# Performance work log

Measured on AMD Instinct MI355X. Metric: run time of the kernel, lower is better.

## Reference

```python
import jax, jax.numpy as jnp
import numpy as np

N_NODES = 50000
N_EDGES = 800000
IN_DIM, HID, EMB = 128, 256, 128


def _gcn_conv(x, src, dst, W, b, n_nodes):
    # PyG GCNConv: add self-loops, symmetric norm D^-1/2 (A+I) D^-1/2, then linear.
    h = x @ W  # [N, out]
    deg = jnp.zeros((n_nodes,), x.dtype).at[dst].add(1.0) + 1.0  # +1 for self-loop
    dinv = jax.lax.rsqrt(deg)
    norm = dinv[src] * dinv[dst]  # [E]
    agg = jnp.zeros_like(h).at[dst].add(h[src] * norm[:, None])
    agg = agg + h * (dinv * dinv)[:, None]  # self-loop term
    return agg + b


def setup_inputs() -> dict:
    key = jax.random.key(0)
    ks = jax.random.split(key, 16)
    s = lambda *sh: None
    x = jax.random.normal(ks[0], (N_NODES, IN_DIM), jnp.float32)
    edge_index = jax.random.randint(ks[1], (2, N_EDGES), 0, N_NODES, jnp.int32)
    def lin(k, fan_in, fan_out):
        lim = 1.0 / np.sqrt(fan_in)
        kw, kb = jax.random.split(k)
        W = jax.random.uniform(kw, (fan_in, fan_out), jnp.float32, -lim, lim)
        b = jax.random.uniform(kb, (fan_out,), jnp.float32, -lim, lim)
        return W, b
    W1, b1 = lin(ks[2], IN_DIM, HID)
    W2, b2 = lin(ks[3], HID, EMB)
    fc1_W, fc1_b = lin(ks[4], EMB, HID)
    fc2_W, fc2_b = lin(ks[5], HID, 1)
    np_W, np_b = lin(ks[6], EMB, 3)
    ep_W, ep_b = lin(ks[7], 2 * EMB, 2)
    gp_W, gp_b = lin(ks[8], EMB, 1)
    return dict(x=x, edge_index=edge_index, W1=W1, b1=b1, W2=W2, b2=b2,
                fc1_W=fc1_W, fc1_b=fc1_b, fc2_W=fc2_W, fc2_b=fc2_b,
                np_W=np_W, np_b=np_b, ep_W=ep_W, ep_b=ep_b, gp_W=gp_W, gp_b=gp_b)


def reference(x, edge_index, W1, b1, W2, b2, fc1_W, fc1_b, fc2_W, fc2_b,
              np_W, np_b, ep_W, ep_b, gp_W, gp_b):
    src, dst = edge_index[0], edge_index[1]
    n = x.shape[0]
    h = jax.nn.relu(_gcn_conv(x, src, dst, W1, b1, n))
    h = jax.nn.relu(_gcn_conv(h, src, dst, W2, b2, n))  # [N, EMB]
    g = jnp.mean(h, axis=0, keepdims=True)  # [1, EMB]
    v = jax.nn.relu(g @ fc1_W + fc1_b)
    value = v @ fc2_W + fc2_b  # [1,1]
    node_logits = h @ np_W + np_b  # [N,3]
    edge_features = jnp.concatenate([h[src], h[dst]], axis=1)  # [E, 2*EMB]
    edge_logits = edge_features @ ep_W + ep_b  # [E,2]
    global_logits = g @ gp_W + gp_b  # [1,1]
    return (node_logits, edge_logits, global_logits, value)
```

## Files before the change

kernel.cpp:

```cpp
#include <hip/hip_runtime.h>
#include <hip/hip_bf16.h>

typedef __attribute__((ext_vector_type(8))) short bf16x8;
typedef __attribute__((ext_vector_type(4))) float f32x4;

__device__ inline unsigned short f2bf(float f) {
    union { float f; unsigned u; } v; v.f = f;
    unsigned r = v.u + 0x7fff + ((v.u >> 16) & 1);
    return (unsigned short)(r >> 16);
}
__device__ inline float bf2f(unsigned short b) {
    union { unsigned u; float f; } v; v.u = ((unsigned)b) << 16;
    return v.f;
}
__device__ inline float bfu_lo(unsigned r) {
    union { unsigned u; float f; } v; v.u = r << 16;
    return v.f;
}
__device__ inline float bfu_hi(unsigned r) {
    union { unsigned u; float f; } v; v.u = r & 0xffff0000u;
    return v.f;
}

__global__ __launch_bounds__(256) void prep_kernel(
    const float* __restrict__ x, unsigned short* __restrict__ xb,
    const float* __restrict__ W1, unsigned short* __restrict__ W1t_hi, unsigned short* __restrict__ W1t_lo,
    const float* __restrict__ W2, unsigned short* __restrict__ W2t_hi, unsigned short* __restrict__ W2t_lo,
    int* __restrict__ zero_ints, float* __restrict__ gsum, int n) {
    int tid = blockIdx.x * blockDim.x + threadIdx.x;
    int C = n * 32;
    if (tid < C) {
        int base = tid * 4;
        float4 v = *(const float4*)&x[base];
        unsigned lo = (unsigned)f2bf(v.x) | ((unsigned)f2bf(v.y) << 16);
        unsigned hi = (unsigned)f2bf(v.z) | ((unsigned)f2bf(v.w) << 16);
        uint2 p; p.x = lo; p.y = hi;
        *(uint2*)&xb[base] = p;
        return;
    }
    tid -= C;
    if (tid < 65536) {
        if (tid < 32768) {
            int k = tid >> 8, j = tid & 255;
            float v = W1[tid];
            unsigned short h = f2bf(v);
            W1t_hi[(size_t)j * 128 + k] = h;
            W1t_lo[(size_t)j * 128 + k] = f2bf(v - bf2f(h));
        } else {
            int i2 = tid - 32768;
            int k = i2 >> 7, j = i2 & 127;
            float v = W2[i2];
            unsigned short h = f2bf(v);
            W2t_hi[(size_t)j * 256 + k] = h;
            W2t_lo[(size_t)j * 256 + k] = f2bf(v - bf2f(h));
        }
        return;
    }
    tid -= 65536;
    if (tid < 2 * n) { zero_ints[tid] = 0; return; }
    tid -= 2 * n;
    if (tid < 128) gsum[tid] = 0.f;
}

__global__ void hist_kernel(const int* __restrict__ dst, int* __restrict__ deg, int nE) {
    int e = blockIdx.x * blockDim.x + threadIdx.x;
    if (e < nE) atomicAdd(&deg[dst[e]], 1);
}

__global__ __launch_bounds__(1024) void scanA_kernel(const int* __restrict__ deg,
                                                     int* __restrict__ local,
                                                     float* __restrict__ dinv,
                                                     int* __restrict__ bsum, int n) {
    __shared__ int wsum[16];
    __shared__ int woff[16];
    int t = threadIdx.x, lane = t & 63, wid = t >> 6;
    int i = blockIdx.x * 1024 + t;
    int val = (i < n) ? deg[i] : 0;
    if (i < n) dinv[i] = rsqrtf((float)(val + 1));
    int inc = val;
    for (int s = 1; s < 64; s <<= 1) {
        int tmp = __shfl_up(inc, s);
        if (lane >= s) inc += tmp;
    }
    if (lane == 63) wsum[wid] = inc;
    __syncthreads();
    if (wid == 0) {
        int w = (lane < 16) ? wsum[lane] : 0;
        for (int s = 1; s < 16; s <<= 1) {
            int tmp = __shfl_up(w, s);
            if (lane >= s) w += tmp;
        }
        if (lane < 16) woff[lane] = w - wsum[lane];
        if (lane == 15) bsum[blockIdx.x] = w;
    }
    __syncthreads();
    if (i < n) local[i] = woff[wid] + (inc - val);
}

__global__ void scanB_kernel(const int* __restrict__ bsum, int* __restrict__ boff, int nb) {
    int lane = threadIdx.x & 63;
    int v = (lane < nb) ? bsum[lane] : 0;
    int inc = v;
    for (int s = 1; s < 64; s <<= 1) {
        int tmp = __shfl_up(inc, s);
        if (lane >= s) inc += tmp;
    }
    if (lane < nb) boff[lane] = inc - v;
}

__global__ void fill_kernel(const int* __restrict__ src, const int* __restrict__ dst,
                            const int* __restrict__ local, const int* __restrict__ boff,
                            int* __restrict__ cnt, const float* __restrict__ dinv,
                            int2* __restrict__ csr, int nE) {
    int e = blockIdx.x * blockDim.x + threadIdx.x;
    if (e >= nE) return;
    int s = src[e], d = dst[e];
    int pos = local[d] + boff[d >> 10] + atomicAdd(&cnt[d], 1);
    float w = dinv[s] * dinv[d];
    csr[pos] = make_int2(s, __float_as_int(w));
}

__global__ __launch_bounds__(256) void gather1_kernel(const unsigned int* __restrict__ xb,
                                                      const int2* __restrict__ csr,
                                                      const int* __restrict__ local,
                                                      const int* __restrict__ boff,
                                                      const int* __restrict__ deg,
                                                      const float* __restrict__ dinv,
                                                      unsigned int* __restrict__ xin_hi,
                                                      unsigned int* __restrict__ xin_lo, int n) {
    int node = blockIdx.x * 4 + (threadIdx.x >> 6);
    int lane = threadIdx.x & 63;
    if (node >= n) return;
    int p = local[node] + boff[node >> 10];
    int e0 = p + deg[node];
    unsigned rs = xb[(size_t)node * 64 + lane];
    float a0 = 0.f, a1 = 0.f, b0 = 0.f, b1 = 0.f;
    float c0 = 0.f, c1 = 0.f, d0v = 0.f, d1v = 0.f;
    for (; p + 7 < e0; p += 8) {
        int2 q0 = csr[p], q1 = csr[p + 1], q2 = csr[p + 2], q3 = csr[p + 3];
        int2 q4 = csr[p + 4], q5 = csr[p + 5], q6 = csr[p + 6], q7 = csr[p + 7];
        unsigned r0 = xb[(size_t)q0.x * 64 + lane];
        unsigned r1 = xb[(size_t)q1.x * 64 + lane];
        unsigned r2 = xb[(size_t)q2.x * 64 + lane];
        unsigned r3 = xb[(size_t)q3.x * 64 + lane];
        unsigned r4 = xb[(size_t)q4.x * 64 + lane];
        unsigned r5 = xb[(size_t)q5.x * 64 + lane];
        unsigned r6 = xb[(size_t)q6.x * 64 + lane];
        unsigned r7 = xb[(size_t)q7.x * 64 + lane];
        float w0 = __int_as_float(q0.y), w1 = __int_as_float(q1.y);
        float w2 = __int_as_float(q2.y), w3 = __int_as_float(q3.y);
        float w4 = __int_as_float(q4.y), w5 = __int_as_float(q5.y);
        float w6 = __int_as_float(q6.y), w7 = __int_as_float(q7.y);
        a0 += w0 * bfu_lo(r0); a1 += w0 * bfu_hi(r0);
        b0 += w1 * bfu_lo(r1); b1 += w1 * bfu_hi(r1);
        c0 += w2 * bfu_lo(r2); c1 += w2 * bfu_hi(r2);
        d0v += w3 * bfu_lo(r3); d1v += w3 * bfu_hi(r3);
        a0 += w4 * bfu_lo(r4); a1 += w4 * bfu_hi(r4);
        b0 += w5 * bfu_lo(r5); b1 += w5 * bfu_hi(r5);
        c0 += w6 * bfu_lo(r6); c1 += w6 * bfu_hi(r6);
        d0v += w7 * bfu_lo(r7); d1v += w7 * bfu_hi(r7);
    }
    for (; p + 3 < e0; p += 4) {
        int2 q0 = csr[p], q1 = csr[p + 1], q2 = csr[p + 2], q3 = csr[p + 3];
        unsigned r0 = xb[(size_t)q0.x * 64 + lane];
        unsigned r1 = xb[(size_t)q1.x * 64 + lane];
        unsigned r2 = xb[(size_t)q2.x * 64 + lane];
        unsigned r3 = xb[(size_t)q3.x * 64 + lane];
        float w0 = __int_as_float(q0.y), w1 = __int_as_float(q1.y);
        float w2 = __int_as_float(q2.y), w3 = __int_as_float(q3.y);
        a0 += w0 * bfu_lo(r0); a1 += w0 * bfu_hi(r0);
        b0 += w1 * bfu_lo(r1); b1 += w1 * bfu_hi(r1);
        c0 += w2 * bfu_lo(r2); c1 += w2 * bfu_hi(r2);
        d0v += w3 * bfu_lo(r3); d1v += w3 * bfu_hi(r3);
    }
    for (; p < e0; ++p) {
        int2 q = csr[p];
        float w = __int_as_float(q.y);
        unsigned r = xb[(size_t)q.x * 64 + lane];
        a0 += w * bfu_lo(r); a1 += w * bfu_hi(r);
    }
    a0 = (a0 + b0) + (c0 + d0v);
    a1 = (a1 + b1) + (c1 + d1v);
    float di = dinv[node];
    float d2 = di * di;
    a0 += d2 * bfu_lo(rs);
    a1 += d2 * bfu_hi(rs);
    unsigned short h0 = f2bf(a0), h1 = f2bf(a1);
    xin_hi[(size_t)node * 64 + lane] = (unsigned)h0 | ((unsigned)h1 << 16);
    unsigned short l0 = f2bf(a0 - bf2f(h0)), l1 = f2bf(a1 - bf2f(h1));
    xin_lo[(size_t)node * 64 + lane] = (unsigned)l0 | ((unsigned)l1 << 16);
}

template <int K, int NOUT, bool BIAS_RELU, bool A_SPLIT>
__global__ __launch_bounds__(256) void mfma_gemm_kernel(
    const unsigned short* __restrict__ Ahi, const unsigned short* __restrict__ Alo,
    const unsigned short* __restrict__ Wthi, const unsigned short* __restrict__ Wtlo,
    const float* __restrict__ bias,
    unsigned short* __restrict__ O, int n) {
    int w = threadIdx.x >> 6, l = threadIdx.x & 63;
    int m0 = blockIdx.x * 128 + w * 32;
    int j0 = blockIdx.y * 64;
    int col16 = l & 15;
    int koff = (l >> 4) * 8;
    int rowA0 = m0 + col16;       if (rowA0 >= n) rowA0 = n - 1;
    int rowA1 = m0 + 16 + col16;  if (rowA1 >= n) rowA1 = n - 1;
    f32x4 acc[2][4];
#pragma unroll
    for (int g = 0; g < 2; ++g)
#pragma unroll
        for (int c = 0; c < 4; ++c) acc[g][c] = (f32x4){0.f, 0.f, 0.f, 0.f};
    for (int k0 = 0; k0 < K; k0 += 32) {
        bf16x8 ah0 = *(const bf16x8*)&Ahi[(size_t)rowA0 * K + k0 + koff];
        bf16x8 ah1 = *(const bf16x8*)&Ahi[(size_t)rowA1 * K + k0 + koff];
        bf16x8 al0, al1;
        if (A_SPLIT) {
            al0 = *(const bf16x8*)&Alo[(size_t)rowA0 * K + k0 + koff];
            al1 = *(const bf16x8*)&Alo[(size_t)rowA1 * K + k0 + koff];
        }
#pragma unroll
        for (int c = 0; c < 4; ++c) {
            size_t wb = (size_t)(j0 + c * 16 + col16) * K + k0 + koff;
            bf16x8 wh = *(const bf16x8*)&Wthi[wb];
            bf16x8 wl = *(const bf16x8*)&Wtlo[wb];
            acc[0][c] = __builtin_amdgcn_mfma_f32_16x16x32_bf16(ah0, wh, acc[0][c], 0, 0, 0);
            if (A_SPLIT) acc[0][c] = __builtin_amdgcn_mfma_f32_16x16x32_bf16(al0, wh, acc[0][c], 0, 0, 0);
            acc[0][c] = __builtin_amdgcn_mfma_f32_16x16x32_bf16(ah0, wl, acc[0][c], 0, 0, 0);
            acc[1][c] = __builtin_amdgcn_mfma_f32_16x16x32_bf16(ah1, wh, acc[1][c], 0, 0, 0);
            if (A_SPLIT) acc[1][c] = __builtin_amdgcn_mfma_f32_16x16x32_bf16(al1, wh, acc[1][c], 0, 0, 0);
            acc[1][c] = __builtin_amdgcn_mfma_f32_16x16x32_bf16(ah1, wl, acc[1][c], 0, 0, 0);
        }
    }
#pragma unroll
    for (int g = 0; g < 2; ++g) {
#pragma unroll
        for (int c = 0; c < 4; ++c) {
            int col = j0 + c * 16 + col16;
#pragma unroll
            for (int r = 0; r < 4; ++r) {
                int orow = m0 + g * 16 + (l >> 4) * 4 + r;
                if (orow >= n) continue;
                float v = acc[g][c][r];
                if (BIAS_RELU) v = fmaxf(v + bias[col], 0.f);
                O[(size_t)orow * NOUT + col] = f2bf(v);
            }
        }
    }
}

__global__ __launch_bounds__(256) void conv2_fused_kernel(
    const unsigned int* __restrict__ h2b, const int2* __restrict__ csr,
    const int* __restrict__ local, const int* __restrict__ boff,
    const int* __restrict__ deg,
    const float* __restrict__ dinv, const float* __restrict__ b2,
    const float* __restrict__ npW, const float* __restrict__ npb,
    const float* __restrict__ epW, const float* __restrict__ epb,
    float* __restrict__ out_nl, float* __restrict__ uv,
    float* __restrict__ gsum, int n) {
    __shared__ float lgs[4][128];
    int lane = threadIdx.x & 63;
    int wid = threadIdx.x >> 6;
    int d0 = lane * 2, d1 = lane * 2 + 1;
    float wn00 = npW[d0 * 3 + 0], wn10 = npW[d0 * 3 + 1], wn20 = npW[d0 * 3 + 2];
    float wn01 = npW[d1 * 3 + 0], wn11 = npW[d1 * 3 + 1], wn21 = npW[d1 * 3 + 2];
    float wu00 = epW[d0 * 2 + 0], wu10 = epW[d0 * 2 + 1];
    float wu01 = epW[d1 * 2 + 0], wu11 = epW[d1 * 2 + 1];
    float wv00 = epW[(d0 + 128) * 2 + 0], wv10 = epW[(d0 + 128) * 2 + 1];
    float wv01 = epW[(d1 + 128) * 2 + 0], wv11 = epW[(d1 + 128) * 2 + 1];
    float b20 = b2[d0], b21 = b2[d1];
    float npb0 = npb[0], npb1 = npb[1], npb2 = npb[2];
    float epb0 = epb[0], epb1 = epb[1];
    float p0 = 0.f, p1 = 0.f;

    for (int node = blockIdx.x * 4 + wid; node < n; node += gridDim.x * 4) {
        int p = local[node] + boff[node >> 10];
        int e0 = p + deg[node];
        unsigned rs = h2b[(size_t)node * 64 + lane];
        float a0 = 0.f, a1 = 0.f, b0 = 0.f, b1 = 0.f;
        float c0 = 0.f, c1 = 0.f, e0v = 0.f, e1v = 0.f;
        for (; p + 7 < e0; p += 8) {
            int2 q0 = csr[p], q1 = csr[p + 1], q2 = csr[p + 2], q3 = csr[p + 3];
            int2 q4 = csr[p + 4], q5 = csr[p + 5], q6 = csr[p + 6], q7 = csr[p + 7];
            unsigned r0 = h2b[(size_t)q0.x * 64 + lane];
            unsigned r1 = h2b[(size_t)q1.x * 64 + lane];
            unsigned r2 = h2b[(size_t)q2.x * 64 + lane];
            unsigned r3 = h2b[(size_t)q3.x * 64 + lane];
            unsigned r4 = h2b[(size_t)q4.x * 64 + lane];
            unsigned r5 = h2b[(size_t)q5.x * 64 + lane];
            unsigned r6 = h2b[(size_t)q6.x * 64 + lane];
            unsigned r7 = h2b[(size_t)q7.x * 64 + lane];
            float w0 = __int_as_float(q0.y), w1 = __int_as_float(q1.y);
            float w2 = __int_as_float(q2.y), w3 = __int_as_float(q3.y);
            float w4 = __int_as_float(q4.y), w5 = __int_as_float(q5.y);
            float w6 = __int_as_float(q6.y), w7 = __int_as_float(q7.y);
            a0 += w0 * bfu_lo(r0); a1 += w0 * bfu_hi(r0);
            b0 += w1 * bfu_lo(r1); b1 += w1 * bfu_hi(r1);
            c0 += w2 * bfu_lo(r2); c1 += w2 * bfu_hi(r2);
            e0v += w3 * bfu_lo(r3); e1v += w3 * bfu_hi(r3);
            a0 += w4 * bfu_lo(r4); a1 += w4 * bfu_hi(r4);
            b0 += w5 * bfu_lo(r5); b1 += w5 * bfu_hi(r5);
            c0 += w6 * bfu_lo(r6); c1 += w6 * bfu_hi(r6);
            e0v += w7 * bfu_lo(r7); e1v += w7 * bfu_hi(r7);
        }
        for (; p + 3 < e0; p += 4) {
            int2 q0 = csr[p], q1 = csr[p + 1], q2 = csr[p + 2], q3 = csr[p + 3];
            unsigned r0 = h2b[(size_t)q0.x * 64 + lane];
            unsigned r1 = h2b[(size_t)q1.x * 64 + lane];
            unsigned r2 = h2b[(size_t)q2.x * 64 + lane];
            unsigned r3 = h2b[(size_t)q3.x * 64 + lane];
            float w0 = __int_as_float(q0.y), w1 = __int_as_float(q1.y);
            float w2 = __int_as_float(q2.y), w3 = __int_as_float(q3.y);
            a0 += w0 * bfu_lo(r0); a1 += w0 * bfu_hi(r0);
            b0 += w1 * bfu_lo(r1); b1 += w1 * bfu_hi(r1);
            c0 += w2 * bfu_lo(r2); c1 += w2 * bfu_hi(r2);
            e0v += w3 * bfu_lo(r3); e1v += w3 * bfu_hi(r3);
        }
        for (; p < e0; ++p) {
            int2 q = csr[p];
            float w = __int_as_float(q.y);
            unsigned r = h2b[(size_t)q.x * 64 + lane];
            a0 += w * bfu_lo(r); a1 += w * bfu_hi(r);
        }
        a0 = (a0 + b0) + (c0 + e0v);
        a1 = (a1 + b1) + (c1 + e1v);
        float di = dinv[node];
        float d2 = di * di;
        a0 = fmaxf(a0 + d2 * bfu_lo(rs) + b20, 0.f);
        a1 = fmaxf(a1 + d2 * bfu_hi(rs) + b21, 0.f);
        p0 += a0;
        p1 += a1;
        float n0 = a0 * wn00 + a1 * wn01;
        float n1 = a0 * wn10 + a1 * wn11;
        float n2 = a0 * wn20 + a1 * wn21;
        float u0 = a0 * wu00 + a1 * wu01;
        float u1 = a0 * wu10 + a1 * wu11;
        float v0 = a0 * wv00 + a1 * wv01;
        float v1 = a0 * wv10 + a1 * wv11;
        for (int off = 32; off; off >>= 1) {
            n0 += __shfl_xor(n0, off);
            n1 += __shfl_xor(n1, off);
            n2 += __shfl_xor(n2, off);
            u0 += __shfl_xor(u0, off);
            u1 += __shfl_xor(u1, off);
            v0 += __shfl_xor(v0, off);
            v1 += __shfl_xor(v1, off);
        }
        if (lane == 0) {
            out_nl[(size_t)node * 3 + 0] = n0 + npb0;
            out_nl[(size_t)node * 3 + 1] = n1 + npb1;
            out_nl[(size_t)node * 3 + 2] = n2 + npb2;
            float4 o;
            o.x = u0 + epb0; o.y = u1 + epb1; o.z = v0; o.w = v1;
            *(float4*)&uv[(size_t)node * 4] = o;
        }
    }
    lgs[wid][d0] = p0;
    lgs[wid][d1] = p1;
    __syncthreads();
    int t = threadIdx.x;
    if (t < 128) {
        float tot = lgs[0][t] + lgs[1][t] + lgs[2][t] + lgs[3][t];
        atomicAdd(&gsum[t], tot);
    }
}

__global__ __launch_bounds__(256) void edge_head_kernel(
    const float* __restrict__ uv, const int* __restrict__ src, const int* __restrict__ dst,
    float* __restrict__ out_el, int nE,
    const float* __restrict__ gsum,
    const float* __restrict__ fc1W, const float* __restrict__ fc1b,
    const float* __restrict__ fc2W, const float* __restrict__ fc2b,
    const float* __restrict__ gpW, const float* __restrict__ gpb,
    float* __restrict__ out_gl, float* __restrict__ out_val, int n) {
    if (blockIdx.x == 0) {
        __shared__ float g[128];
        __shared__ float red[256];
        int t = threadIdx.x;
        if (t < 128) g[t] = gsum[t] * (1.0f / (float)n);
        __syncthreads();
        float v = fc1b[t];
#pragma unroll
        for (int k = 0; k < 128; ++k) v += g[k] * fc1W[k * 256 + t];
        v = fmaxf(v, 0.0f);
        red[t] = v * fc2W[t];
        __syncthreads();
        for (int s = 128; s > 0; s >>= 1) { if (t < s) red[t] += red[t + s]; __syncthreads(); }
        if (t == 0) out_val[0] = red[0] + fc2b[0];
        __syncthreads();
        red[t] = (t < 128) ? g[t] * gpW[t] : 0.0f;
        __syncthreads();
        for (int s = 128; s > 0; s >>= 1) { if (t < s) red[t] += red[t + s]; __syncthreads(); }
        if (t == 0) out_gl[0] = red[0] + gpb[0];
        return;
    }
    int e = (blockIdx.x - 1) * blockDim.x + threadIdx.x;
    if (e >= nE) return;
    int s = src[e], d = dst[e];
    float2 u = *(const float2*)&uv[(size_t)s * 4];
    float2 v = *(const float2*)&uv[(size_t)d * 4 + 2];
    float2 o; o.x = u.x + v.x; o.y = u.y + v.y;
    *(float2*)&out_el[(size_t)e * 2] = o;
}

extern "C" void kernel_launch(void* const* d_in, const int* in_sizes, int n_in,
                              void* d_out, int out_size, void* d_ws, size_t ws_size,
                              hipStream_t stream) {
    const float* x    = (const float*)d_in[0];
    const int*   ei   = (const int*)d_in[1];
    const float* W1   = (const float*)d_in[2];
    const float* b1   = (const float*)d_in[3];
    const float* W2   = (const float*)d_in[4];
    const float* b2   = (const float*)d_in[5];
    const float* fc1W = (const float*)d_in[6];
    const float* fc1b = (const float*)d_in[7];
    const float* fc2W = (const float*)d_in[8];
    const float* fc2b = (const float*)d_in[9];
    const float* npW  = (const float*)d_in[10];
    const float* npb  = (const float*)d_in[11];
    const float* epW  = (const float*)d_in[12];
    const float* epb  = (const float*)d_in[13];
    const float* gpW  = (const float*)d_in[14];
    const float* gpb  = (const float*)d_in[15];
    float* out = (float*)d_out;

    const int n = in_sizes[0] / 128;
    const int E = in_sizes[1] / 2;
    const int* src = ei;
    const int* dst = ei + E;
    const int nb = (n + 1023) / 1024;

    char* p = (char*)d_ws;
    auto alloc = [&](size_t bytes) { char* r = p; p += (bytes + 255) & ~(size_t)255; return r; };
    unsigned short* xb     = (unsigned short*)alloc((size_t)n * 128 * 2);
    unsigned short* xin_hi = (unsigned short*)alloc((size_t)n * 128 * 2);
    unsigned short* xin_lo = (unsigned short*)alloc((size_t)n * 128 * 2);
    unsigned short* h      = (unsigned short*)alloc((size_t)n * 256 * 2);
    unsigned short* W1t_hi = (unsigned short*)alloc(128 * 256 * 2);
    unsigned short* W1t_lo = (unsigned short*)alloc(128 * 256 * 2);
    unsigned short* W2t_hi = (unsigned short*)alloc(256 * 128 * 2);
    unsigned short* W2t_lo = (unsigned short*)alloc(256 * 128 * 2);
    int2*  csr    = (int2*)alloc((size_t)E * 8);
    int*   deg    = (int*)alloc((size_t)n * 4 * 2);
    int*   cnt    = deg + n;
    int*   local  = (int*)alloc((size_t)n * 4);
    int*   bsum   = (int*)alloc(64 * 4);
    int*   boff   = (int*)alloc(64 * 4);
    float* dinv   = (float*)alloc((size_t)n * 4);
    float* uv     = (float*)alloc((size_t)n * 16);
    float* gsum   = (float*)alloc(512);
    unsigned short* h2b = xb;

    float* out_nl  = out;
    float* out_el  = out + (size_t)n * 3;
    float* out_gl  = out + (size_t)n * 3 + (size_t)E * 2;
    float* out_val = out_gl + 1;

    {
        long total = (long)n * 32 + 65536 + 2L * n + 128;
        int blocks = (int)((total + 255) / 256);
        prep_kernel<<<blocks, 256, 0, stream>>>(x, xb, W1, W1t_hi, W1t_lo,
                                                W2, W2t_hi, W2t_lo, deg, gsum, n);
    }

    hist_kernel<<<(E + 255) / 256, 256, 0, stream>>>(dst, deg, E);
    scanA_kernel<<<nb, 1024, 0, stream>>>(deg, local, dinv, bsum, n);
    scanB_kernel<<<1, 64, 0, stream>>>(bsum, boff, nb);
    fill_kernel<<<(E + 255) / 256, 256, 0, stream>>>(src, dst, local, boff, cnt, dinv, csr, E);

    gather1_kernel<<<(n + 3) / 4, 256, 0, stream>>>((const unsigned int*)xb, csr, local, boff,
                                                    deg, dinv, (unsigned int*)xin_hi,
                                                    (unsigned int*)xin_lo, n);

    dim3 g1((n + 127) / 128, 256 / 64);
    mfma_gemm_kernel<128, 256, true, true><<<g1, 256, 0, stream>>>(xin_hi, xin_lo, W1t_hi, W1t_lo,
                                                                   b1, h, n);
    dim3 g2((n + 127) / 128, 128 / 64);
    mfma_gemm_kernel<256, 128, false, false><<<g2, 256, 0, stream>>>(h, nullptr, W2t_hi, W2t_lo,
                                                                     nullptr, h2b, n);

    conv2_fused_kernel<<<2048, 256, 0, stream>>>((const unsigned int*)h2b, csr, local, boff,
                                                 deg, dinv, b2, npW, npb, epW, epb,
                                                 out_nl, uv, gsum, n);

    edge_head_kernel<<<1 + (E + 255) / 256, 256, 0, stream>>>(uv, src, dst, out_el, E,
                                                              gsum, fc1W, fc1b, fc2W, fc2b,
                                                              gpW, gpb, out_gl, out_val, n);
}
```

Before: 407.1 us.

## Fold degree histogram into prep kernel, memset buffers, shrink GEMM row tile

Result: slower. 436.1 us (+7.1%).

```diff
diff --git a/kernel.cpp b/kernel.cpp
--- a/kernel.cpp
+++ b/kernel.cpp
@@ -26,7 +26,7 @@
     const float* __restrict__ x, unsigned short* __restrict__ xb,
     const float* __restrict__ W1, unsigned short* __restrict__ W1t_hi, unsigned short* __restrict__ W1t_lo,
     const float* __restrict__ W2, unsigned short* __restrict__ W2t_hi, unsigned short* __restrict__ W2t_lo,
-    int* __restrict__ zero_ints, float* __restrict__ gsum, int n) {
+    const int* __restrict__ dst, int* __restrict__ deg, int n, int E) {
     int tid = blockIdx.x * blockDim.x + threadIdx.x;
     int C = n * 32;
     if (tid < C) {
@@ -57,14 +57,7 @@
         return;
     }
     tid -= 65536;
-    if (tid < 2 * n) { zero_ints[tid] = 0; return; }
-    tid -= 2 * n;
-    if (tid < 128) gsum[tid] = 0.f;
-}
-
-__global__ void hist_kernel(const int* __restrict__ dst, int* __restrict__ deg, int nE) {
-    int e = blockIdx.x * blockDim.x + threadIdx.x;
-    if (e < nE) atomicAdd(&deg[dst[e]], 1);
+    if (tid < E) atomicAdd(&deg[dst[tid]], 1);
 }
 
 __global__ __launch_bounds__(1024) void scanA_kernel(const int* __restrict__ deg,
@@ -198,51 +191,39 @@
     const float* __restrict__ bias,
     unsigned short* __restrict__ O, int n) {
     int w = threadIdx.x >> 6, l = threadIdx.x & 63;
-    int m0 = blockIdx.x * 128 + w * 32;
+    int m0 = blockIdx.x * 64 + w * 16;
     int j0 = blockIdx.y * 64;
     int col16 = l & 15;
     int koff = (l >> 4) * 8;
-    int rowA0 = m0 + col16;       if (rowA0 >= n) rowA0 = n - 1;
-    int rowA1 = m0 + 16 + col16;  if (rowA1 >= n) rowA1 = n - 1;
-    f32x4 acc[2][4];
+    int rowA = m0 + col16;
+    if (rowA >= n) rowA = n - 1;
+    f32x4 acc[4];
 #pragma unroll
-    for (int g = 0; g < 2; ++g)
-#pragma unroll
-        for (int c = 0; c < 4; ++c) acc[g][c] = (f32x4){0.f, 0.f, 0.f, 0.f};
+    for (int c = 0; c < 4; ++c) acc[c] = (f32x4){0.f, 0.f, 0.f, 0.f};
     for (int k0 = 0; k0 < K; k0 += 32) {
-        bf16x8 ah0 = *(const bf16x8*)&Ahi[(size_t)rowA0 * K + k0 + koff];
-        bf16x8 ah1 = *(const bf16x8*)&Ahi[(size_t)rowA1 * K + k0 + koff];
-        bf16x8 al0, al1;
-        if (A_SPLIT) {
-            al0 = *(const bf16x8*)&Alo[(size_t)rowA0 * K + k0 + koff];
-            al1 = *(const bf16x8*)&Alo[(size_t)rowA1 * K + k0 + koff];
-        }
+        bf16x8 ah = *(const bf16x8*)&Ahi[(size_t)rowA * K + k0 + koff];
+        bf16x8 al;
+        if (A_SPLIT) al = *(const bf16x8*)&Alo[(size_t)rowA * K + k0 + koff];
 #pragma unroll
         for (int c = 0; c < 4; ++c) {
             size_t wb = (size_t)(j0 + c * 16 + col16) * K + k0 + koff;
             bf16x8 wh = *(const bf16x8*)&Wthi[wb];
             bf16x8 wl = *(const bf16x8*)&Wtlo[wb];
-            acc[0][c] = __builtin_amdgcn_mfma_f32_16x16x32_bf16(ah0, wh, acc[0][c], 0, 0, 0);
-            if (A_SPLIT) acc[0][c] = __builtin_amdgcn_mfma_f32_16x16x32_bf16(al0, wh, acc[0][c], 0, 0, 0);
-            acc[0][c] = __builtin_amdgcn_mfma_f32_16x16x32_bf16(ah0, wl, acc[0][c], 0, 0, 0);
-            acc[1][c] = __builtin_amdgcn_mfma_f32_16x16x32_bf16(ah1, wh, acc[1][c], 0, 0, 0);
-            if (A_SPLIT) acc[1][c] = __builtin_amdgcn_mfma_f32_16x16x32_bf16(al1, wh, acc[1][c], 0, 0, 0);
-            acc[1][c] = __builtin_amdgcn_mfma_f32_16x16x32_bf16(ah1, wl, acc[1][c], 0, 0, 0);
+            acc[c] = __builtin_amdgcn_mfma_f32_16x16x32_bf16(ah, wh, acc[c], 0, 0, 0);
+            if (A_SPLIT) acc[c] = __builtin_amdgcn_mfma_f32_16x16x32_bf16(al, wh, acc[c], 0, 0, 0);
+            acc[c] = __builtin_amdgcn_mfma_f32_16x16x32_bf16(ah, wl, acc[c], 0, 0, 0);
         }
     }
 #pragma unroll
-    for (int g = 0; g < 2; ++g) {
+    for (int c = 0; c < 4; ++c) {
+        int col = j0 + c * 16 + col16;
 #pragma unroll
-        for (int c = 0; c < 4; ++c) {
-            int col = j0 + c * 16 + col16;
-#pragma unroll
-            for (int r = 0; r < 4; ++r) {
-                int orow = m0 + g * 16 + (l >> 4) * 4 + r;
-                if (orow >= n) continue;
-                float v = acc[g][c][r];
-                if (BIAS_RELU) v = fmaxf(v + bias[col], 0.f);
-                O[(size_t)orow * NOUT + col] = f2bf(v);
-            }
+        for (int r = 0; r < 4; ++r) {
+            int orow = m0 + (l >> 4) * 4 + r;
+            if (orow >= n) continue;
+            float v = acc[c][r];
+            if (BIAS_RELU) v = fmaxf(v + bias[col], 0.f);
+            O[(size_t)orow * NOUT + col] = f2bf(v);
         }
     }
 }
@@ -454,14 +435,16 @@
     float* out_gl  = out + (size_t)n * 3 + (size_t)E * 2;
     float* out_val = out_gl + 1;
 
+    hipMemsetAsync(deg, 0, (size_t)2 * n * sizeof(int), stream);
+    hipMemsetAsync(gsum, 0, 128 * sizeof(float), stream);
+
     {
-        long total = (long)n * 32 + 65536 + 2L * n + 128;
+        long total = (long)n * 32 + 65536 + (long)E;
         int blocks = (int)((total + 255) / 256);
         prep_kernel<<<blocks, 256, 0, stream>>>(x, xb, W1, W1t_hi, W1t_lo,
-                                                W2, W2t_hi, W2t_lo, deg, gsum, n);
-    }
-
-    hist_kernel<<<(E + 255) / 256, 256, 0, stream>>>(dst, deg, E);
+                                                W2, W2t_hi, W2t_lo, dst, deg, n, E);
+    }
+
     scanA_kernel<<<nb, 1024, 0, stream>>>(deg, local, dinv, bsum, n);
     scanB_kernel<<<1, 64, 0, stream>>>(bsum, boff, nb);
     fill_kernel<<<(E + 255) / 256, 256, 0, stream>>>(src, dst, local, boff, cnt, dinv, csr, E);
@@ -470,10 +453,10 @@
                                                     deg, dinv, (unsigned int*)xin_hi,
                                                     (unsigned int*)xin_lo, n);
 
-    dim3 g1((n + 127) / 128, 256 / 64);
+    dim3 g1((n + 63) / 64, 4);
     mfma_gemm_kernel<128, 256, true, true><<<g1, 256, 0, stream>>>(xin_hi, xin_lo, W1t_hi, W1t_lo,
                                                                    b1, h, n);
-    dim3 g2((n + 127) / 128, 128 / 64);
+    dim3 g2((n + 63) / 64, 2);
     mfma_gemm_kernel<256, 128, false, false><<<g2, 256, 0, stream>>>(h, nullptr, W2t_hi, W2t_lo,
                                                                      nullptr, h2b, n);
 
```
